# Optimization experiments

Measured on AMD Instinct MI355X. Metric: run time of the kernel, lower is better.

## Reference

```python
import jax, jax.numpy as jnp
import numpy as np
import math

QK_DIM = 128

def setup_inputs() -> dict:
    key = jax.random.key(0)
    kx, kq, kk, kv = jax.random.split(key, 4)
    B, S, D, H = 4, 4096, 1024, 128
    X = jax.random.normal(kx, (B, S, D), dtype=jnp.float32)
    # xavier-normal-ish scale for weights
    std = math.sqrt(2.0 / (D + H))
    W_q = jax.random.normal(kq, (D, H), dtype=jnp.float32) * std
    W_k = jax.random.normal(kk, (D, H), dtype=jnp.float32) * std
    W_v = jax.random.normal(kv, (D, H), dtype=jnp.float32) * std
    return {"X": X, "W_q": W_q, "W_k": W_k, "W_v": W_v}

def reference(X, W_q, W_k, W_v):
    # X: [B, S, D]; single-head causal attention
    Q = X @ W_q                       # [B, S, H]
    K = X @ W_k                       # [B, S, H]
    V = X @ W_v                       # [B, S, H]
    S_len = X.shape[1]
    scores = jnp.einsum('bsh,bth->bst', Q, K) / math.sqrt(QK_DIM)  # [B, S, S]
    causal = jnp.tril(jnp.ones((S_len, S_len), dtype=bool))
    scores = jnp.where(causal, scores, -jnp.inf)
    attn = jax.nn.softmax(scores, axis=-1)
    return jnp.einsum('bst,bth->bsh', attn, V)
```

## Files before the change

kernel.cpp:

```cpp
#include <hip/hip_runtime.h>
#include <hip/hip_bf16.h>

#define B_ 4
#define S_ 4096
#define D_ 1024
#define H_ 128

typedef unsigned short u16;
typedef unsigned int u32;
typedef short s16x8 __attribute__((ext_vector_type(8)));
typedef float f32x4 __attribute__((ext_vector_type(4)));

__device__ __forceinline__ u16 f2bf(float f) {
    u32 x = __float_as_uint(f);
    u32 r = x + 0x7fffu + ((x >> 16) & 1u);
    return (u16)(r >> 16);
}

__device__ __forceinline__ void gl_lds16(const u16* g, u16* l) {
    __builtin_amdgcn_global_load_lds(
        (const __attribute__((address_space(1))) u32*)g,
        (__attribute__((address_space(3))) u32*)l, 16, 0, 0);
}

__global__ void detect_dtype_kernel(const u32* __restrict__ w, int* __restrict__ flag) {
    __shared__ int smax[256];
    const int tid = threadIdx.x;
    int m = 0;
    for (int i = tid; i < 1024; i += 256) {
        u32 x = w[i];
        m = max(m, max((int)((x >> 7) & 0xFF), (int)((x >> 23) & 0xFF)));
    }
    smax[tid] = m;
    __syncthreads();
    if (tid == 0) {
        int mm = 0;
        for (int i = 0; i < 256; ++i) mm = max(mm, smax[i]);
        *flag = (mm >= 200) ? 1 : 0;
    }
}

__global__ __launch_bounds__(256) void prep_w_kernel(
    const void* __restrict__ Wq, const void* __restrict__ Wk, const void* __restrict__ Wv,
    u16* __restrict__ Wt, const int* __restrict__ dflag)
{
    const int kt = blockIdx.x, mat = blockIdx.y;
    const void* W = (mat == 0) ? Wq : (mat == 1) ? Wk : Wv;
    const int isf = *dflag;
    const int t = threadIdx.x;
    const int kk = t >> 3;
    const int n0 = (t & 7) * 16;
    u16 vals[16];
    if (isf) {
        const float* wp = (const float*)W + (size_t)(kt * 32 + kk) * H_ + n0;
#pragma unroll
        for (int i = 0; i < 16; ++i) vals[i] = f2bf(wp[i]);
    } else {
        const u16* wp = (const u16*)W + (size_t)(kt * 32 + kk) * H_ + n0;
#pragma unroll
        for (int i = 0; i < 16; ++i) vals[i] = wp[i];
    }
    const size_t base = (size_t)(mat * 32 + kt) * 128;
#pragma unroll
    for (int i = 0; i < 16; ++i)
        Wt[(base + n0 + i) * 32 + kk] = vals[i];
}

__global__ __launch_bounds__(256) void qkv_kernel(
    const void* __restrict__ Xv, const u16* __restrict__ Wt,
    u16* __restrict__ Qo, u16* __restrict__ Ko, u16* __restrict__ Vto,
    const int* __restrict__ dflag)
{
    __shared__ u16 Ws[2][384 * 32];
    __shared__ union { u16 qk[32 * 136]; u16 vt[128 * 40]; } OsU;

    const int isf = *dflag;
    const int tid = threadIdx.x;
    const int w = tid >> 6, lane = tid & 63;
    const int r = lane & 15, q = lane >> 4;
    const size_t m0 = (size_t)blockIdx.x * 32;

    f32x4 acc[2][6];
#pragma unroll
    for (int s2 = 0; s2 < 2; ++s2)
#pragma unroll
        for (int i = 0; i < 6; ++i) acc[s2][i] = (f32x4){0.f, 0.f, 0.f, 0.f};

    const float* xf0 = (const float*)Xv + (m0 + r) * D_;
    const float* xf1 = (const float*)Xv + (m0 + 16 + r) * D_;
    const u16*   xb0 = (const u16*)Xv + (m0 + r) * D_;
    const u16*   xb1 = (const u16*)Xv + (m0 + 16 + r) * D_;

    float4 af[2][2];
    uint4  ab[2];

#pragma unroll
    for (int i = 0; i < 6; ++i) {
        int c = tid + i * 256;
        gl_lds16(Wt + (size_t)((c >> 9) * 32) * 4096 + (c & 511) * 8, &Ws[0][c * 8]);
    }
    if (isf) {
        af[0][0] = *(const float4*)(xf0 + q * 8);
        af[0][1] = *(const float4*)(xf0 + q * 8 + 4);
        af[1][0] = *(const float4*)(xf1 + q * 8);
        af[1][1] = *(const float4*)(xf1 + q * 8 + 4);
    } else {
        ab[0] = *(const uint4*)(xb0 + q * 8);
        ab[1] = *(const uint4*)(xb1 + q * 8);
    }

    for (int kt = 0; kt < 32; ++kt) {
        const int buf = kt & 1;
        __syncthreads();

        if (kt + 1 < 32) {
#pragma unroll
            for (int i = 0; i < 6; ++i) {
                int c = tid + i * 256;
                gl_lds16(Wt + (size_t)((c >> 9) * 32 + kt + 1) * 4096 + (c & 511) * 8,
                         &Ws[buf ^ 1][c * 8]);
            }
        }

        s16x8 a[2];
        if (isf) {
#pragma unroll
            for (int s2 = 0; s2 < 2; ++s2) {
                union { u16 u[8]; s16x8 v; } pk;
                pk.u[0] = f2bf(af[s2][0].x); pk.u[1] = f2bf(af[s2][0].y);
                pk.u[2] = f2bf(af[s2][0].z); pk.u[3] = f2bf(af[s2][0].w);
                pk.u[4] = f2bf(af[s2][1].x); pk.u[5] = f2bf(af[s2][1].y);
                pk.u[6] = f2bf(af[s2][1].z); pk.u[7] = f2bf(af[s2][1].w);
                a[s2] = pk.v;
            }
        } else {
            a[0] = *(const s16x8*)&ab[0];
            a[1] = *(const s16x8*)&ab[1];
        }

        if (kt + 1 < 32) {
            const int k0 = (kt + 1) * 32;
            if (isf) {
                af[0][0] = *(const float4*)(xf0 + k0 + q * 8);
                af[0][1] = *(const float4*)(xf0 + k0 + q * 8 + 4);
                af[1][0] = *(const float4*)(xf1 + k0 + q * 8);
                af[1][1] = *(const float4*)(xf1 + k0 + q * 8 + 4);
            } else {
                ab[0] = *(const uint4*)(xb0 + k0 + q * 8);
                ab[1] = *(const uint4*)(xb1 + k0 + q * 8);
            }
        }

#pragma unroll
        for (int i = 0; i < 6; ++i) {
            int c = w * 6 + i;
            s16x8 b = *(const s16x8*)&Ws[buf][(c >> 3) * 4096 + ((c & 7) * 16 + r) * 32 + q * 8];
            acc[0][i] = __builtin_amdgcn_mfma_f32_16x16x32_bf16(a[0], b, acc[0][i], 0, 0, 0);
            acc[1][i] = __builtin_amdgcn_mfma_f32_16x16x32_bf16(a[1], b, acc[1][i], 0, 0, 0);
        }
    }

    u16* outs[2] = {Qo, Ko};
    for (int m = 0; m < 2; ++m) {
        const float sc = (m == 0) ? 0.08838834764831845f : 1.0f;
        __syncthreads();
#pragma unroll
        for (int i = 0; i < 6; ++i) {
            int c = w * 6 + i;
            if ((c >> 3) == m) {
                int nt = c & 7;
#pragma unroll
                for (int s2 = 0; s2 < 2; ++s2)
#pragma unroll
                    for (int reg = 0; reg < 4; ++reg)
                        OsU.qk[(s2 * 16 + q * 4 + reg) * 136 + nt * 16 + r] = f2bf(acc[s2][i][reg] * sc);
            }
        }
        __syncthreads();
        u16* Out = outs[m];
#pragma unroll
        for (int it = 0; it < 2; ++it) {
            int c = tid + it * 256;
            int row = c >> 4, col = (c & 15) * 8;
            *(uint4*)(Out + (m0 + row) * H_ + col) = *(const uint4*)&OsU.qk[row * 136 + col];
        }
    }

    __syncthreads();
#pragma unroll
    for (int i = 0; i < 6; ++i) {
        int c = w * 6 + i;
        if ((c >> 3) == 2) {
            int nt = c & 7;
#pragma unroll
            for (int s2 = 0; s2 < 2; ++s2)
#pragma unroll
                for (int reg = 0; reg < 4; ++reg)
                    OsU.vt[(nt * 16 + r) * 40 + s2 * 16 + q * 4 + reg] = f2bf(acc[s2][i][reg]);
        }
    }
    __syncthreads();
    {
        const int bb = blockIdx.x >> 7;
        const int s0 = (blockIdx.x & 127) * 32;
#pragma unroll
        for (int it = 0; it < 2; ++it) {
            int c = tid + it * 256;
            int h = c >> 2, sh = (c & 3) * 8;
            *(uint4*)(Vto + ((size_t)bb * H_ + h) * S_ + s0 + sh) =
                *(const uint4*)&OsU.vt[h * 40 + sh];
        }
    }
}

__global__ __launch_bounds__(256) void attn_kernel(
    const u16* __restrict__ Q, const u16* __restrict__ K, const u16* __restrict__ Vt,
    void* __restrict__ out, const int* __restrict__ dflag)
{
    __shared__ union {
        u16 ps[2][32 * 136];
        float of[32 * 132];
    } U;
    __shared__ float lsumS[4][32];

    const int isf = *dflag;
    const int tid = threadIdx.x;
    const int w = tid >> 6, lane = tid & 63;
    const int r = lane & 15, q = lane >> 4;
    const int bid = blockIdx.x;
    const int b = bid & 3;
    const int qt = (bid < 256) ? (bid >> 2) : (127 - ((bid - 256) >> 2));

    const u16* Qg  = Q  + ((size_t)b * S_ + (size_t)qt * 32) * H_;
    const u16* Kg  = K  + (size_t)b * S_ * H_;
    const u16* Vtg = Vt + (size_t)b * H_ * S_;

    s16x8 qf[2][4];
#pragma unroll
    for (int M = 0; M < 2; ++M)
#pragma unroll
        for (int ks = 0; ks < 4; ++ks)
            qf[M][ks] = *(const s16x8*)(Qg + (size_t)(M * 16 + r) * H_ + ks * 32 + q * 8);

    float lp[2][4];
#pragma unroll
    for (int M = 0; M < 2; ++M)
#pragma unroll
        for (int reg = 0; reg < 4; ++reg) lp[M][reg] = 0.f;

    f32x4 accO[2][2];
#pragma unroll
    for (int M = 0; M < 2; ++M)
#pragma unroll
        for (int ht = 0; ht < 2; ++ht) accO[M][ht] = (f32x4){0.f, 0.f, 0.f, 0.f};

    const int nKT = (qt >> 2) + 1;

    s16x8 kf[2][4];
#pragma unroll
    for (int t2 = 0; t2 < 2; ++t2)
#pragma unroll
        for (int ks = 0; ks < 4; ++ks)
            kf[t2][ks] = *(const s16x8*)(Kg + (size_t)(w * 32 + t2 * 16 + r) * H_ + ks * 32 + q * 8);

    for (int j = 0; j < nKT; ++j) {
        f32x4 accS[2][2];
#pragma unroll
        for (int M = 0; M < 2; ++M)
#pragma unroll
            for (int t2 = 0; t2 < 2; ++t2) accS[M][t2] = (f32x4){0.f, 0.f, 0.f, 0.f};
#pragma unroll
        for (int ks = 0; ks < 4; ++ks)
#pragma unroll
            for (int t2 = 0; t2 < 2; ++t2)
#pragma unroll
                for (int M = 0; M < 2; ++M)
                    accS[M][t2] = __builtin_amdgcn_mfma_f32_16x16x32_bf16(qf[M][ks], kf[t2][ks], accS[M][t2], 0, 0, 0);

        s16x8 vf[2][4];
#pragma unroll
        for (int ht = 0; ht < 2; ++ht)
#pragma unroll
            for (int ks = 0; ks < 4; ++ks)
                vf[ht][ks] = *(const s16x8*)(Vtg + (size_t)(w * 32 + ht * 16 + r) * S_ + (size_t)j * 128 + ks * 32 + q * 8);

        const bool last = (j == nKT - 1);
        const int key0 = j * 128 + w * 32 + r;
        u16* psb = &U.ps[j & 1][0];
#pragma unroll
        for (int M = 0; M < 2; ++M)
#pragma unroll
            for (int t2 = 0; t2 < 2; ++t2)
#pragma unroll
                for (int reg = 0; reg < 4; ++reg) {
                    int key = key0 + t2 * 16;
                    int grow = qt * 32 + M * 16 + q * 4 + reg;
                    float s = fminf(accS[M][t2][reg], 80.f);
                    float p = __expf(s);
                    if (last && key > grow) p = 0.f;
                    lp[M][reg] += p;
                    psb[(M * 16 + q * 4 + reg) * 136 + w * 32 + t2 * 16 + r] = f2bf(p);
                }
        __syncthreads();

        if (j + 1 < nKT) {
#pragma unroll
            for (int t2 = 0; t2 < 2; ++t2)
#pragma unroll
                for (int ks = 0; ks < 4; ++ks)
                    kf[t2][ks] = *(const s16x8*)(Kg + ((size_t)(j + 1) * 128 + w * 32 + t2 * 16 + r) * H_ + ks * 32 + q * 8);
        }

#pragma unroll
        for (int ks = 0; ks < 4; ++ks) {
            s16x8 pa0 = *(const s16x8*)&psb[(size_t)(r) * 136 + ks * 32 + q * 8];
            s16x8 pa1 = *(const s16x8*)&psb[(size_t)(16 + r) * 136 + ks * 32 + q * 8];
#pragma unroll
            for (int ht = 0; ht < 2; ++ht) {
                accO[0][ht] = __builtin_amdgcn_mfma_f32_16x16x32_bf16(pa0, vf[ht][ks], accO[0][ht], 0, 0, 0);
                accO[1][ht] = __builtin_amdgcn_mfma_f32_16x16x32_bf16(pa1, vf[ht][ks], accO[1][ht], 0, 0, 0);
            }
        }
    }

#pragma unroll
    for (int M = 0; M < 2; ++M)
#pragma unroll
        for (int reg = 0; reg < 4; ++reg) {
            float v = lp[M][reg];
            v += __shfl_xor(v, 1);
            v += __shfl_xor(v, 2);
            v += __shfl_xor(v, 4);
            v += __shfl_xor(v, 8);
            lp[M][reg] = v;
        }
    if (r == 0) {
#pragma unroll
        for (int M = 0; M < 2; ++M)
#pragma unroll
            for (int reg = 0; reg < 4; ++reg)
                lsumS[w][M * 16 + q * 4 + reg] = lp[M][reg];
    }
    __syncthreads();

    float linv[2][4];
#pragma unroll
    for (int M = 0; M < 2; ++M)
#pragma unroll
        for (int reg = 0; reg < 4; ++reg) {
            int row = M * 16 + q * 4 + reg;
            linv[M][reg] = 1.0f / (lsumS[0][row] + lsumS[1][row] + lsumS[2][row] + lsumS[3][row]);
        }

#pragma unroll
    for (int M = 0; M < 2; ++M)
#pragma unroll
        for (int ht = 0; ht < 2; ++ht)
#pragma unroll
            for (int reg = 0; reg < 4; ++reg)
                U.of[(M * 16 + q * 4 + reg) * 132 + w * 32 + ht * 16 + r] = accO[M][ht][reg] * linv[M][reg];
    __syncthreads();
    {
        const size_t obase = (size_t)b * S_ + (size_t)qt * 32;
        int row = tid >> 3, col = (tid & 7) * 16;
        const float* src = &U.of[row * 132 + col];
        if (isf) {
            float* dst = (float*)out + (obase + row) * H_ + col;
#pragma unroll
            for (int i = 0; i < 4; ++i)
                *(float4*)(dst + i * 4) = *(const float4*)(src + i * 4);
        } else {
            u16* dst = (u16*)out + (obase + row) * H_ + col;
#pragma unroll
            for (int hh = 0; hh < 2; ++hh) {
                union { u16 u[8]; uint4 v; } pk;
#pragma unroll
                for (int i = 0; i < 8; ++i) pk.u[i] = f2bf(src[hh * 8 + i]);
                *(uint4*)(dst + hh * 8) = pk.v;
            }
        }
    }
}

extern "C" void kernel_launch(void* const* d_in, const int* in_sizes, int n_in,
                              void* d_out, int out_size, void* d_ws, size_t ws_size,
                              hipStream_t stream) {
    (void)in_sizes; (void)n_in; (void)out_size; (void)ws_size;
    const void* X  = d_in[0];
    const void* Wq = d_in[1];
    const void* Wk = d_in[2];
    const void* Wv = d_in[3];

    int* dflag = (int*)d_ws;
    u16* Qw = (u16*)((char*)d_ws + 256);
    const size_t n = (size_t)B_ * S_ * H_;
    u16* Kw = Qw + n;
    u16* Vtw = Kw + n;
    u16* Wt = Vtw + n;

    detect_dtype_kernel<<<1, 256, 0, stream>>>((const u32*)Wq, dflag);
    prep_w_kernel<<<dim3(32, 3), 256, 0, stream>>>(Wq, Wk, Wv, Wt, dflag);
    qkv_kernel<<<512, 256, 0, stream>>>(X, Wt, Qw, Kw, Vtw, dflag);
    attn_kernel<<<512, 256, 0, stream>>>(Qw, Kw, Vtw, d_out, dflag);
}
```

Baseline: 213.0 us.

## Widen attention blocks to 8 waves processing 256-key tiles per iteration

The attention kernel now launches 512 threads (8 waves) per block and walks the keys in 256-wide tiles instead of 128. Each wave computes scores for 32 keys and owns a 16-column slice of the 128-wide head dimension for the PV product. This halves the number of loop iterations and block-wide barriers per query tile and puts more waves per CU. The cost is a larger LDS probability buffer, a register cap from launch_bounds(512,4), and more masked-out work in the last causal tile.

```diff
diff --git a/kernel.cpp b/kernel.cpp
--- a/kernel.cpp
+++ b/kernel.cpp
@@ -213,15 +213,15 @@
     }
 }
 
-__global__ __launch_bounds__(256) void attn_kernel(
+__global__ __launch_bounds__(512, 4) void attn_kernel(
     const u16* __restrict__ Q, const u16* __restrict__ K, const u16* __restrict__ Vt,
     void* __restrict__ out, const int* __restrict__ dflag)
 {
     __shared__ union {
-        u16 ps[2][32 * 136];
+        u16 ps[2][32 * 264];
         float of[32 * 132];
     } U;
-    __shared__ float lsumS[4][32];
+    __shared__ float lsumS[8][32];
 
     const int isf = *dflag;
     const int tid = threadIdx.x;
@@ -248,13 +248,11 @@
 #pragma unroll
         for (int reg = 0; reg < 4; ++reg) lp[M][reg] = 0.f;
 
-    f32x4 accO[2][2];
-#pragma unroll
-    for (int M = 0; M < 2; ++M)
-#pragma unroll
-        for (int ht = 0; ht < 2; ++ht) accO[M][ht] = (f32x4){0.f, 0.f, 0.f, 0.f};
-
-    const int nKT = (qt >> 2) + 1;
+    f32x4 accO[2];
+#pragma unroll
+    for (int M = 0; M < 2; ++M) accO[M] = (f32x4){0.f, 0.f, 0.f, 0.f};
+
+    const int nKT = (qt >> 3) + 1;
 
     s16x8 kf[2][4];
 #pragma unroll
@@ -277,15 +275,13 @@
                 for (int M = 0; M < 2; ++M)
                     accS[M][t2] = __builtin_amdgcn_mfma_f32_16x16x32_bf16(qf[M][ks], kf[t2][ks], accS[M][t2], 0, 0, 0);
 
-        s16x8 vf[2][4];
-#pragma unroll
-        for (int ht = 0; ht < 2; ++ht)
-#pragma unroll
-            for (int ks = 0; ks < 4; ++ks)
-                vf[ht][ks] = *(const s16x8*)(Vtg + (size_t)(w * 32 + ht * 16 + r) * S_ + (size_t)j * 128 + ks * 32 + q * 8);
+        s16x8 vf[8];
+#pragma unroll
+        for (int ks = 0; ks < 8; ++ks)
+            vf[ks] = *(const s16x8*)(Vtg + (size_t)(w * 16 + r) * S_ + (size_t)j * 256 + ks * 32 + q * 8);
 
         const bool last = (j == nKT - 1);
-        const int key0 = j * 128 + w * 32 + r;
+        const int key0 = j * 256 + w * 32 + r;
         u16* psb = &U.ps[j & 1][0];
 #pragma unroll
         for (int M = 0; M < 2; ++M)
@@ -299,7 +295,7 @@
                     float p = __expf(s);
                     if (last && key > grow) p = 0.f;
                     lp[M][reg] += p;
-                    psb[(M * 16 + q * 4 + reg) * 136 + w * 32 + t2 * 16 + r] = f2bf(p);
+                    psb[(M * 16 + q * 4 + reg) * 264 + w * 32 + t2 * 16 + r] = f2bf(p);
                 }
         __syncthreads();
 
@@ -308,18 +304,15 @@
             for (int t2 = 0; t2 < 2; ++t2)
 #pragma unroll
                 for (int ks = 0; ks < 4; ++ks)
-                    kf[t2][ks] = *(const s16x8*)(Kg + ((size_t)(j + 1) * 128 + w * 32 + t2 * 16 + r) * H_ + ks * 32 + q * 8);
-        }
-
-#pragma unroll
-        for (int ks = 0; ks < 4; ++ks) {
-            s16x8 pa0 = *(const s16x8*)&psb[(size_t)(r) * 136 + ks * 32 + q * 8];
-            s16x8 pa1 = *(const s16x8*)&psb[(size_t)(16 + r) * 136 + ks * 32 + q * 8];
-#pragma unroll
-            for (int ht = 0; ht < 2; ++ht) {
-                accO[0][ht] = __builtin_amdgcn_mfma_f32_16x16x32_bf16(pa0, vf[ht][ks], accO[0][ht], 0, 0, 0);
-                accO[1][ht] = __builtin_amdgcn_mfma_f32_16x16x32_bf16(pa1, vf[ht][ks], accO[1][ht], 0, 0, 0);
-            }
+                    kf[t2][ks] = *(const s16x8*)(Kg + ((size_t)(j + 1) * 256 + w * 32 + t2 * 16 + r) * H_ + ks * 32 + q * 8);
+        }
+
+#pragma unroll
+        for (int ks = 0; ks < 8; ++ks) {
+            s16x8 pa0 = *(const s16x8*)&psb[(size_t)(r) * 264 + ks * 32 + q * 8];
+            s16x8 pa1 = *(const s16x8*)&psb[(size_t)(16 + r) * 264 + ks * 32 + q * 8];
+            accO[0] = __builtin_amdgcn_mfma_f32_16x16x32_bf16(pa0, vf[ks], accO[0], 0, 0, 0);
+            accO[1] = __builtin_amdgcn_mfma_f32_16x16x32_bf16(pa1, vf[ks], accO[1], 0, 0, 0);
         }
     }
 
@@ -349,35 +342,33 @@
 #pragma unroll
         for (int reg = 0; reg < 4; ++reg) {
             int row = M * 16 + q * 4 + reg;
-            linv[M][reg] = 1.0f / (lsumS[0][row] + lsumS[1][row] + lsumS[2][row] + lsumS[3][row]);
-        }
-
-#pragma unroll
-    for (int M = 0; M < 2; ++M)
-#pragma unroll
-        for (int ht = 0; ht < 2; ++ht)
-#pragma unroll
-            for (int reg = 0; reg < 4; ++reg)
-                U.of[(M * 16 + q * 4 + reg) * 132 + w * 32 + ht * 16 + r] = accO[M][ht][reg] * linv[M][reg];
+            float s = 0.f;
+#pragma unroll
+            for (int ww = 0; ww < 8; ++ww) s += lsumS[ww][row];
+            linv[M][reg] = 1.0f / s;
+        }
+
+#pragma unroll
+    for (int M = 0; M < 2; ++M)
+#pragma unroll
+        for (int reg = 0; reg < 4; ++reg)
+            U.of[(M * 16 + q * 4 + reg) * 132 + w * 16 + r] = accO[M][reg] * linv[M][reg];
     __syncthreads();
     {
         const size_t obase = (size_t)b * S_ + (size_t)qt * 32;
-        int row = tid >> 3, col = (tid & 7) * 16;
+        int row = tid >> 4, col = (tid & 15) * 8;
         const float* src = &U.of[row * 132 + col];
         if (isf) {
             float* dst = (float*)out + (obase + row) * H_ + col;
 #pragma unroll
-            for (int i = 0; i < 4; ++i)
+            for (int i = 0; i < 2; ++i)
                 *(float4*)(dst + i * 4) = *(const float4*)(src + i * 4);
         } else {
             u16* dst = (u16*)out + (obase + row) * H_ + col;
-#pragma unroll
-            for (int hh = 0; hh < 2; ++hh) {
-                union { u16 u[8]; uint4 v; } pk;
-#pragma unroll
-                for (int i = 0; i < 8; ++i) pk.u[i] = f2bf(src[hh * 8 + i]);
-                *(uint4*)(dst + hh * 8) = pk.v;
-            }
+            union { u16 u[8]; uint4 v; } pk;
+#pragma unroll
+            for (int i = 0; i < 8; ++i) pk.u[i] = f2bf(src[i]);
+            *(uint4*)dst = pk.v;
         }
     }
 }
@@ -401,5 +392,5 @@
     detect_dtype_kernel<<<1, 256, 0, stream>>>((const u32*)Wq, dflag);
     prep_w_kernel<<<dim3(32, 3), 256, 0, stream>>>(Wq, Wk, Wv, Wt, dflag);
     qkv_kernel<<<512, 256, 0, stream>>>(X, Wt, Qw, Kw, Vtw, dflag);
-    attn_kernel<<<512, 256, 0, stream>>>(Qw, Kw, Vtw, d_out, dflag);
-}
+    attn_kernel<<<512, 512, 0, stream>>>(Qw, Kw, Vtw, d_out, dflag);
+}
```

Result: slower. 242.2 us (+13.7%).

## Split causal attention into balanced key-range chunks with separate combine kernel

Applied to the files above, without the earlier changes.

Replaces the single attention kernel with a split-K scheme. Each block handles a paired short/long query tile over one of four key-tile ranges, so every block does roughly the same amount of work. Unnormalized fp32 partial outputs and row sums go to workspace, and a new combine kernel sums them and normalizes. The aim is better load balance and more blocks (1024) across the CUs. The cost is extra global traffic for the fp32 partials, plus one more kernel launch.

```diff
diff --git a/kernel.cpp b/kernel.cpp
--- a/kernel.cpp
+++ b/kernel.cpp
@@ -213,171 +213,216 @@
     }
 }
 
-__global__ __launch_bounds__(256) void attn_kernel(
+__global__ __launch_bounds__(256) void attn_partial_kernel(
     const u16* __restrict__ Q, const u16* __restrict__ K, const u16* __restrict__ Vt,
-    void* __restrict__ out, const int* __restrict__ dflag)
+    float* __restrict__ OP, float* __restrict__ LP)
 {
-    __shared__ union {
-        u16 ps[2][32 * 136];
-        float of[32 * 132];
-    } U;
+    __shared__ u16 ps[2][32 * 136];
     __shared__ float lsumS[4][32];
 
-    const int isf = *dflag;
     const int tid = threadIdx.x;
     const int w = tid >> 6, lane = tid & 63;
     const int r = lane & 15, q = lane >> 4;
     const int bid = blockIdx.x;
     const int b = bid & 3;
-    const int qt = (bid < 256) ? (bid >> 2) : (127 - ((bid - 256) >> 2));
-
-    const u16* Qg  = Q  + ((size_t)b * S_ + (size_t)qt * 32) * H_;
+    const int c = (bid >> 2) & 3;
+    const int p = bid >> 4;
+    const int nA = (p >> 2) + 1;
+    const int s_c = (c == 0) ? 0 : (8 * c + 1);
+    const int e_c = 8 * c + 9;
+
     const u16* Kg  = K  + (size_t)b * S_ * H_;
     const u16* Vtg = Vt + (size_t)b * H_ * S_;
 
-    s16x8 qf[2][4];
-#pragma unroll
-    for (int M = 0; M < 2; ++M)
-#pragma unroll
-        for (int ks = 0; ks < 4; ++ks)
-            qf[M][ks] = *(const s16x8*)(Qg + (size_t)(M * 16 + r) * H_ + ks * 32 + q * 8);
-
-    float lp[2][4];
-#pragma unroll
-    for (int M = 0; M < 2; ++M)
-#pragma unroll
-        for (int reg = 0; reg < 4; ++reg) lp[M][reg] = 0.f;
-
-    f32x4 accO[2][2];
-#pragma unroll
-    for (int M = 0; M < 2; ++M)
-#pragma unroll
-        for (int ht = 0; ht < 2; ++ht) accO[M][ht] = (f32x4){0.f, 0.f, 0.f, 0.f};
-
-    const int nKT = (qt >> 2) + 1;
-
-    s16x8 kf[2][4];
-#pragma unroll
-    for (int t2 = 0; t2 < 2; ++t2)
-#pragma unroll
-        for (int ks = 0; ks < 4; ++ks)
-            kf[t2][ks] = *(const s16x8*)(Kg + (size_t)(w * 32 + t2 * 16 + r) * H_ + ks * 32 + q * 8);
-
-    for (int j = 0; j < nKT; ++j) {
-        f32x4 accS[2][2];
+    for (int seg = 0; seg < 2; ++seg) {
+        int qt, jlo, jhi;
+        if (seg == 0) {
+            if (s_c >= nA) continue;
+            qt = p; jlo = s_c; jhi = min(e_c, nA);
+        } else {
+            if (e_c <= nA) continue;
+            qt = 127 - p; jlo = max(s_c, nA) - nA; jhi = e_c - nA;
+        }
+        const int nQT = (qt >> 2) + 1;
+        const u16* Qg = Q + ((size_t)b * S_ + (size_t)qt * 32) * H_;
+
+        s16x8 qf[2][4];
 #pragma unroll
         for (int M = 0; M < 2; ++M)
 #pragma unroll
-            for (int t2 = 0; t2 < 2; ++t2) accS[M][t2] = (f32x4){0.f, 0.f, 0.f, 0.f};
-#pragma unroll
-        for (int ks = 0; ks < 4; ++ks)
-#pragma unroll
-            for (int t2 = 0; t2 < 2; ++t2)
-#pragma unroll
-                for (int M = 0; M < 2; ++M)
-                    accS[M][t2] = __builtin_amdgcn_mfma_f32_16x16x32_bf16(qf[M][ks], kf[t2][ks], accS[M][t2], 0, 0, 0);
-
-        s16x8 vf[2][4];
-#pragma unroll
-        for (int ht = 0; ht < 2; ++ht)
-#pragma unroll
             for (int ks = 0; ks < 4; ++ks)
-                vf[ht][ks] = *(const s16x8*)(Vtg + (size_t)(w * 32 + ht * 16 + r) * S_ + (size_t)j * 128 + ks * 32 + q * 8);
-
-        const bool last = (j == nKT - 1);
-        const int key0 = j * 128 + w * 32 + r;
-        u16* psb = &U.ps[j & 1][0];
+                qf[M][ks] = *(const s16x8*)(Qg + (size_t)(M * 16 + r) * H_ + ks * 32 + q * 8);
+
+        float lp[2][4];
 #pragma unroll
         for (int M = 0; M < 2; ++M)
 #pragma unroll
-            for (int t2 = 0; t2 < 2; ++t2)
-#pragma unroll
-                for (int reg = 0; reg < 4; ++reg) {
-                    int key = key0 + t2 * 16;
-                    int grow = qt * 32 + M * 16 + q * 4 + reg;
-                    float s = fminf(accS[M][t2][reg], 80.f);
-                    float p = __expf(s);
-                    if (last && key > grow) p = 0.f;
-                    lp[M][reg] += p;
-                    psb[(M * 16 + q * 4 + reg) * 136 + w * 32 + t2 * 16 + r] = f2bf(p);
+            for (int reg = 0; reg < 4; ++reg) lp[M][reg] = 0.f;
+
+        f32x4 accO[2][2];
+#pragma unroll
+        for (int M = 0; M < 2; ++M)
+#pragma unroll
+            for (int ht = 0; ht < 2; ++ht) accO[M][ht] = (f32x4){0.f, 0.f, 0.f, 0.f};
+
+        s16x8 kf[2][4];
+#pragma unroll
+        for (int t2 = 0; t2 < 2; ++t2)
+#pragma unroll
+            for (int ks = 0; ks < 4; ++ks)
+                kf[t2][ks] = *(const s16x8*)(Kg + ((size_t)jlo * 128 + w * 32 + t2 * 16 + r) * H_ + ks * 32 + q * 8);
+
+        for (int j = jlo; j < jhi; ++j) {
+            f32x4 accS[2][2];
+#pragma unroll
+            for (int M = 0; M < 2; ++M)
+#pragma unroll
+                for (int t2 = 0; t2 < 2; ++t2) accS[M][t2] = (f32x4){0.f, 0.f, 0.f, 0.f};
+#pragma unroll
+            for (int ks = 0; ks < 4; ++ks)
+#pragma unroll
+                for (int t2 = 0; t2 < 2; ++t2)
+#pragma unroll
+                    for (int M = 0; M < 2; ++M)
+                        accS[M][t2] = __builtin_amdgcn_mfma_f32_16x16x32_bf16(qf[M][ks], kf[t2][ks], accS[M][t2], 0, 0, 0);
+
+            s16x8 vf[2][4];
+#pragma unroll
+            for (int ht = 0; ht < 2; ++ht)
+#pragma unroll
+                for (int ks = 0; ks < 4; ++ks)
+                    vf[ht][ks] = *(const s16x8*)(Vtg + (size_t)(w * 32 + ht * 16 + r) * S_ + (size_t)j * 128 + ks * 32 + q * 8);
+
+            const bool last = (j == nQT - 1);
+            const int key0 = j * 128 + w * 32 + r;
+            u16* psb = &ps[j & 1][0];
+#pragma unroll
+            for (int M = 0; M < 2; ++M)
+#pragma unroll
+                for (int t2 = 0; t2 < 2; ++t2)
+#pragma unroll
+                    for (int reg = 0; reg < 4; ++reg) {
+                        int key = key0 + t2 * 16;
+                        int grow = qt * 32 + M * 16 + q * 4 + reg;
+                        float s = fminf(accS[M][t2][reg], 80.f);
+                        float pv = __expf(s);
+                        if (last && key > grow) pv = 0.f;
+                        lp[M][reg] += pv;
+                        psb[(M * 16 + q * 4 + reg) * 136 + w * 32 + t2 * 16 + r] = f2bf(pv);
+                    }
+            __syncthreads();
+
+            if (j + 1 < jhi) {
+#pragma unroll
+                for (int t2 = 0; t2 < 2; ++t2)
+#pragma unroll
+                    for (int ks = 0; ks < 4; ++ks)
+                        kf[t2][ks] = *(const s16x8*)(Kg + ((size_t)(j + 1) * 128 + w * 32 + t2 * 16 + r) * H_ + ks * 32 + q * 8);
+            }
+
+#pragma unroll
+            for (int ks = 0; ks < 4; ++ks) {
+                s16x8 pa0 = *(const s16x8*)&psb[(size_t)(r) * 136 + ks * 32 + q * 8];
+                s16x8 pa1 = *(const s16x8*)&psb[(size_t)(16 + r) * 136 + ks * 32 + q * 8];
+#pragma unroll
+                for (int ht = 0; ht < 2; ++ht) {
+                    accO[0][ht] = __builtin_amdgcn_mfma_f32_16x16x32_bf16(pa0, vf[ht][ks], accO[0][ht], 0, 0, 0);
+                    accO[1][ht] = __builtin_amdgcn_mfma_f32_16x16x32_bf16(pa1, vf[ht][ks], accO[1][ht], 0, 0, 0);
                 }
+            }
+        }
+
+#pragma unroll
+        for (int M = 0; M < 2; ++M)
+#pragma unroll
+            for (int reg = 0; reg < 4; ++reg) {
+                float v = lp[M][reg];
+                v += __shfl_xor(v, 1);
+                v += __shfl_xor(v, 2);
+                v += __shfl_xor(v, 4);
+                v += __shfl_xor(v, 8);
+                lp[M][reg] = v;
+            }
+        if (r == 0) {
+#pragma unroll
+            for (int M = 0; M < 2; ++M)
+#pragma unroll
+                for (int reg = 0; reg < 4; ++reg)
+                    lsumS[w][M * 16 + q * 4 + reg] = lp[M][reg];
+        }
         __syncthreads();
 
-        if (j + 1 < nKT) {
-#pragma unroll
-            for (int t2 = 0; t2 < 2; ++t2)
-#pragma unroll
-                for (int ks = 0; ks < 4; ++ks)
-                    kf[t2][ks] = *(const s16x8*)(Kg + ((size_t)(j + 1) * 128 + w * 32 + t2 * 16 + r) * H_ + ks * 32 + q * 8);
-        }
-
-#pragma unroll
-        for (int ks = 0; ks < 4; ++ks) {
-            s16x8 pa0 = *(const s16x8*)&psb[(size_t)(r) * 136 + ks * 32 + q * 8];
-            s16x8 pa1 = *(const s16x8*)&psb[(size_t)(16 + r) * 136 + ks * 32 + q * 8];
-#pragma unroll
-            for (int ht = 0; ht < 2; ++ht) {
-                accO[0][ht] = __builtin_amdgcn_mfma_f32_16x16x32_bf16(pa0, vf[ht][ks], accO[0][ht], 0, 0, 0);
-                accO[1][ht] = __builtin_amdgcn_mfma_f32_16x16x32_bf16(pa1, vf[ht][ks], accO[1][ht], 0, 0, 0);
-            }
-        }
-    }
-
-#pragma unroll
-    for (int M = 0; M < 2; ++M)
-#pragma unroll
-        for (int reg = 0; reg < 4; ++reg) {
-            float v = lp[M][reg];
-            v += __shfl_xor(v, 1);
-            v += __shfl_xor(v, 2);
-            v += __shfl_xor(v, 4);
-            v += __shfl_xor(v, 8);
-            lp[M][reg] = v;
-        }
-    if (r == 0) {
+        const size_t slot = (size_t)(b * 128 + qt) * 4 + c;
+        if (w == 0 && lane < 32)
+            LP[slot * 32 + lane] = lsumS[0][lane] + lsumS[1][lane] + lsumS[2][lane] + lsumS[3][lane];
+
+        float* Os = OP + slot * 32 * 128;
 #pragma unroll
         for (int M = 0; M < 2; ++M)
 #pragma unroll
-            for (int reg = 0; reg < 4; ++reg)
-                lsumS[w][M * 16 + q * 4 + reg] = lp[M][reg];
-    }
-    __syncthreads();
-
-    float linv[2][4];
-#pragma unroll
-    for (int M = 0; M < 2; ++M)
-#pragma unroll
-        for (int reg = 0; reg < 4; ++reg) {
-            int row = M * 16 + q * 4 + reg;
-            linv[M][reg] = 1.0f / (lsumS[0][row] + lsumS[1][row] + lsumS[2][row] + lsumS[3][row]);
-        }
-
-#pragma unroll
-    for (int M = 0; M < 2; ++M)
-#pragma unroll
-        for (int ht = 0; ht < 2; ++ht)
-#pragma unroll
-            for (int reg = 0; reg < 4; ++reg)
-                U.of[(M * 16 + q * 4 + reg) * 132 + w * 32 + ht * 16 + r] = accO[M][ht][reg] * linv[M][reg];
-    __syncthreads();
-    {
-        const size_t obase = (size_t)b * S_ + (size_t)qt * 32;
-        int row = tid >> 3, col = (tid & 7) * 16;
-        const float* src = &U.of[row * 132 + col];
-        if (isf) {
-            float* dst = (float*)out + (obase + row) * H_ + col;
-#pragma unroll
-            for (int i = 0; i < 4; ++i)
-                *(float4*)(dst + i * 4) = *(const float4*)(src + i * 4);
-        } else {
-            u16* dst = (u16*)out + (obase + row) * H_ + col;
-#pragma unroll
-            for (int hh = 0; hh < 2; ++hh) {
-                union { u16 u[8]; uint4 v; } pk;
-#pragma unroll
-                for (int i = 0; i < 8; ++i) pk.u[i] = f2bf(src[hh * 8 + i]);
-                *(uint4*)(dst + hh * 8) = pk.v;
-            }
+            for (int ht = 0; ht < 2; ++ht)
+#pragma unroll
+                for (int reg = 0; reg < 4; ++reg)
+                    Os[(M * 16 + q * 4 + reg) * 128 + w * 32 + ht * 16 + r] = accO[M][ht][reg];
+        __syncthreads();
+    }
+}
+
+__global__ __launch_bounds__(256) void combine_kernel(
+    const float* __restrict__ OP, const float* __restrict__ LP,
+    void* __restrict__ out, const int* __restrict__ dflag)
+{
+    const int isf = *dflag;
+    const int bid = blockIdx.x;
+    const int qt = bid & 127;
+    const int p = (qt < 64) ? qt : 127 - qt;
+    const bool isA = (qt < 64);
+    const int nA = (p >> 2) + 1;
+    const int tid = threadIdx.x;
+    const int row = tid >> 3;
+    const int col = (tid & 7) * 16;
+
+    float4 acc0 = {0, 0, 0, 0}, acc1 = {0, 0, 0, 0}, acc2 = {0, 0, 0, 0}, acc3 = {0, 0, 0, 0};
+    float l = 0.f;
+#pragma unroll
+    for (int c = 0; c < 4; ++c) {
+        const int s_c = (c == 0) ? 0 : (8 * c + 1);
+        const int e_c = 8 * c + 9;
+        const bool valid = isA ? (s_c < nA) : (e_c > nA);
+        if (valid) {
+            const size_t slot = (size_t)bid * 4 + c;
+            const float* Os = OP + (slot * 32 + row) * 128 + col;
+            float4 t0 = *(const float4*)(Os);
+            float4 t1 = *(const float4*)(Os + 4);
+            float4 t2 = *(const float4*)(Os + 8);
+            float4 t3 = *(const float4*)(Os + 12);
+            acc0.x += t0.x; acc0.y += t0.y; acc0.z += t0.z; acc0.w += t0.w;
+            acc1.x += t1.x; acc1.y += t1.y; acc1.z += t1.z; acc1.w += t1.w;
+            acc2.x += t2.x; acc2.y += t2.y; acc2.z += t2.z; acc2.w += t2.w;
+            acc3.x += t3.x; acc3.y += t3.y; acc3.z += t3.z; acc3.w += t3.w;
+            l += LP[slot * 32 + row];
+        }
+    }
+    const float inv = 1.0f / l;
+    float vals[16] = {acc0.x, acc0.y, acc0.z, acc0.w, acc1.x, acc1.y, acc1.z, acc1.w,
+                      acc2.x, acc2.y, acc2.z, acc2.w, acc3.x, acc3.y, acc3.z, acc3.w};
+#pragma unroll
+    for (int i = 0; i < 16; ++i) vals[i] *= inv;
+
+    const size_t orow = (size_t)(bid >> 7) * S_ + (size_t)qt * 32 + row;
+    if (isf) {
+        float* dst = (float*)out + orow * H_ + col;
+#pragma unroll
+        for (int i = 0; i < 4; ++i)
+            *(float4*)(dst + i * 4) = *(const float4*)(&vals[i * 4]);
+    } else {
+        u16* dst = (u16*)out + orow * H_ + col;
+#pragma unroll
+        for (int hh = 0; hh < 2; ++hh) {
+            union { u16 u[8]; uint4 v; } pk;
+#pragma unroll
+            for (int i = 0; i < 8; ++i) pk.u[i] = f2bf(vals[hh * 8 + i]);
+            *(uint4*)(dst + hh * 8) = pk.v;
         }
     }
 }
@@ -397,9 +442,12 @@
     u16* Kw = Qw + n;
     u16* Vtw = Kw + n;
     u16* Wt = Vtw + n;
+    float* OP = (float*)(Wt + 3 * 1024 * 128);
+    float* LP = OP + (size_t)4 * 128 * 4 * 32 * 128;
 
     detect_dtype_kernel<<<1, 256, 0, stream>>>((const u32*)Wq, dflag);
     prep_w_kernel<<<dim3(32, 3), 256, 0, stream>>>(Wq, Wk, Wv, Wt, dflag);
     qkv_kernel<<<512, 256, 0, stream>>>(X, Wt, Qw, Kw, Vtw, dflag);
-    attn_kernel<<<512, 256, 0, stream>>>(Qw, Kw, Vtw, d_out, dflag);
-}
+    attn_partial_kernel<<<1024, 256, 0, stream>>>(Qw, Kw, Vtw, OP, LP);
+    combine_kernel<<<512, 256, 0, stream>>>(OP, LP, d_out, dflag);
+}
```

Result: slower. 224.9 us (+5.6%).

## Pair causal query tiles and split long tiles across blocks with combine pass

Applied to the files above, without the earlier changes.

Replaces the 32-row attention kernel with 512-thread blocks covering 64-row query tiles. Each short tile is paired with its long mirror tile, and the long tile's KV range is split across two blocks so every block does equal work. The split partial outputs and row sums go to workspace in fp32, and a new combine kernel merges and normalizes them. This targets causal load imbalance and tail effects, at the cost of an extra launch, workspace traffic for the partials, and fewer total blocks (256).

```diff
diff --git a/kernel.cpp b/kernel.cpp
--- a/kernel.cpp
+++ b/kernel.cpp
@@ -213,171 +213,257 @@
     }
 }
 
-__global__ __launch_bounds__(256) void attn_kernel(
+__global__ __launch_bounds__(512) void attn_pair_kernel(
     const u16* __restrict__ Q, const u16* __restrict__ K, const u16* __restrict__ Vt,
-    void* __restrict__ out, const int* __restrict__ dflag)
+    void* __restrict__ out, float* __restrict__ OP, float* __restrict__ LP,
+    const int* __restrict__ dflag)
 {
     __shared__ union {
-        u16 ps[2][32 * 136];
-        float of[32 * 132];
+        u16 ps[2][64 * 136];
+        float of[64 * 132];
     } U;
-    __shared__ float lsumS[4][32];
+    __shared__ float lsumS[8][32];
 
     const int isf = *dflag;
     const int tid = threadIdx.x;
     const int w = tid >> 6, lane = tid & 63;
+    const int qh = w >> 2;
+    const int kw = w & 3;
     const int r = lane & 15, q = lane >> 4;
     const int bid = blockIdx.x;
     const int b = bid & 3;
-    const int qt = (bid < 256) ? (bid >> 2) : (127 - ((bid - 256) >> 2));
-
-    const u16* Qg  = Q  + ((size_t)b * S_ + (size_t)qt * 32) * H_;
+    const int p = (bid >> 2) & 31;
+    const int c = bid >> 7;
+    const int qtA = p, qtB = 63 - p;
+    const int nA = (p >> 1) + 1;
+    const int nB = ((63 - p) >> 1) + 1;
+    const int m = 17 - nA;
+
     const u16* Kg  = K  + (size_t)b * S_ * H_;
     const u16* Vtg = Vt + (size_t)b * H_ * S_;
 
-    s16x8 qf[2][4];
-#pragma unroll
-    for (int M = 0; M < 2; ++M)
-#pragma unroll
-        for (int ks = 0; ks < 4; ++ks)
-            qf[M][ks] = *(const s16x8*)(Qg + (size_t)(M * 16 + r) * H_ + ks * 32 + q * 8);
-
-    float lp[2][4];
-#pragma unroll
-    for (int M = 0; M < 2; ++M)
-#pragma unroll
-        for (int reg = 0; reg < 4; ++reg) lp[M][reg] = 0.f;
-
-    f32x4 accO[2][2];
-#pragma unroll
-    for (int M = 0; M < 2; ++M)
-#pragma unroll
-        for (int ht = 0; ht < 2; ++ht) accO[M][ht] = (f32x4){0.f, 0.f, 0.f, 0.f};
-
-    const int nKT = (qt >> 2) + 1;
-
-    s16x8 kf[2][4];
-#pragma unroll
-    for (int t2 = 0; t2 < 2; ++t2)
-#pragma unroll
-        for (int ks = 0; ks < 4; ++ks)
-            kf[t2][ks] = *(const s16x8*)(Kg + (size_t)(w * 32 + t2 * 16 + r) * H_ + ks * 32 + q * 8);
-
-    for (int j = 0; j < nKT; ++j) {
-        f32x4 accS[2][2];
+    for (int seg = 0; seg < 2; ++seg) {
+        int qt, jlo, jhi;
+        bool direct;
+        if (seg == 0) {
+            if (c != 0) continue;
+            qt = qtA; jlo = 0; jhi = nA; direct = true;
+        } else {
+            qt = qtB; jlo = (c == 0) ? 0 : m; jhi = (c == 0) ? m : nB; direct = false;
+        }
+        const int nQT = (qt >> 1) + 1;
+        const u16* Qg = Q + ((size_t)b * S_ + (size_t)qt * 64) * H_;
+
+        s16x8 qf[2][4];
 #pragma unroll
         for (int M = 0; M < 2; ++M)
 #pragma unroll
-            for (int t2 = 0; t2 < 2; ++t2) accS[M][t2] = (f32x4){0.f, 0.f, 0.f, 0.f};
-#pragma unroll
-        for (int ks = 0; ks < 4; ++ks)
-#pragma unroll
-            for (int t2 = 0; t2 < 2; ++t2)
-#pragma unroll
-                for (int M = 0; M < 2; ++M)
-                    accS[M][t2] = __builtin_amdgcn_mfma_f32_16x16x32_bf16(qf[M][ks], kf[t2][ks], accS[M][t2], 0, 0, 0);
-
-        s16x8 vf[2][4];
-#pragma unroll
-        for (int ht = 0; ht < 2; ++ht)
-#pragma unroll
             for (int ks = 0; ks < 4; ++ks)
-                vf[ht][ks] = *(const s16x8*)(Vtg + (size_t)(w * 32 + ht * 16 + r) * S_ + (size_t)j * 128 + ks * 32 + q * 8);
-
-        const bool last = (j == nKT - 1);
-        const int key0 = j * 128 + w * 32 + r;
-        u16* psb = &U.ps[j & 1][0];
+                qf[M][ks] = *(const s16x8*)(Qg + (size_t)(qh * 32 + M * 16 + r) * H_ + ks * 32 + q * 8);
+
+        float lp[2][4];
 #pragma unroll
         for (int M = 0; M < 2; ++M)
 #pragma unroll
-            for (int t2 = 0; t2 < 2; ++t2)
+            for (int reg = 0; reg < 4; ++reg) lp[M][reg] = 0.f;
+
+        f32x4 accO[2][2];
+#pragma unroll
+        for (int M = 0; M < 2; ++M)
+#pragma unroll
+            for (int ht = 0; ht < 2; ++ht) accO[M][ht] = (f32x4){0.f, 0.f, 0.f, 0.f};
+
+        s16x8 kf[2][4];
+#pragma unroll
+        for (int t2 = 0; t2 < 2; ++t2)
+#pragma unroll
+            for (int ks = 0; ks < 4; ++ks)
+                kf[t2][ks] = *(const s16x8*)(Kg + ((size_t)jlo * 128 + kw * 32 + t2 * 16 + r) * H_ + ks * 32 + q * 8);
+
+        for (int j = jlo; j < jhi; ++j) {
+            f32x4 accS[2][2];
+#pragma unroll
+            for (int M = 0; M < 2; ++M)
+#pragma unroll
+                for (int t2 = 0; t2 < 2; ++t2) accS[M][t2] = (f32x4){0.f, 0.f, 0.f, 0.f};
+#pragma unroll
+            for (int ks = 0; ks < 4; ++ks)
+#pragma unroll
+                for (int t2 = 0; t2 < 2; ++t2)
+#pragma unroll
+                    for (int M = 0; M < 2; ++M)
+                        accS[M][t2] = __builtin_amdgcn_mfma_f32_16x16x32_bf16(qf[M][ks], kf[t2][ks], accS[M][t2], 0, 0, 0);
+
+            s16x8 vf[2][4];
+#pragma unroll
+            for (int ht = 0; ht < 2; ++ht)
+#pragma unroll
+                for (int ks = 0; ks < 4; ++ks)
+                    vf[ht][ks] = *(const s16x8*)(Vtg + (size_t)(kw * 32 + ht * 16 + r) * S_ + (size_t)j * 128 + ks * 32 + q * 8);
+
+            const bool last = (j == nQT - 1);
+            const int key0 = j * 128 + kw * 32 + r;
+            u16* psb = &U.ps[j & 1][0];
+#pragma unroll
+            for (int M = 0; M < 2; ++M)
+#pragma unroll
+                for (int t2 = 0; t2 < 2; ++t2)
+#pragma unroll
+                    for (int reg = 0; reg < 4; ++reg) {
+                        int key = key0 + t2 * 16;
+                        int grow = qt * 64 + qh * 32 + M * 16 + q * 4 + reg;
+                        float s = fminf(accS[M][t2][reg], 80.f);
+                        float pv = __expf(s);
+                        if (last && key > grow) pv = 0.f;
+                        lp[M][reg] += pv;
+                        psb[(qh * 32 + M * 16 + q * 4 + reg) * 136 + kw * 32 + t2 * 16 + r] = f2bf(pv);
+                    }
+            __syncthreads();
+
+            if (j + 1 < jhi) {
+#pragma unroll
+                for (int t2 = 0; t2 < 2; ++t2)
+#pragma unroll
+                    for (int ks = 0; ks < 4; ++ks)
+                        kf[t2][ks] = *(const s16x8*)(Kg + ((size_t)(j + 1) * 128 + kw * 32 + t2 * 16 + r) * H_ + ks * 32 + q * 8);
+            }
+
+#pragma unroll
+            for (int ks = 0; ks < 4; ++ks) {
+                s16x8 pa0 = *(const s16x8*)&psb[(size_t)(qh * 32 + r) * 136 + ks * 32 + q * 8];
+                s16x8 pa1 = *(const s16x8*)&psb[(size_t)(qh * 32 + 16 + r) * 136 + ks * 32 + q * 8];
+#pragma unroll
+                for (int ht = 0; ht < 2; ++ht) {
+                    accO[0][ht] = __builtin_amdgcn_mfma_f32_16x16x32_bf16(pa0, vf[ht][ks], accO[0][ht], 0, 0, 0);
+                    accO[1][ht] = __builtin_amdgcn_mfma_f32_16x16x32_bf16(pa1, vf[ht][ks], accO[1][ht], 0, 0, 0);
+                }
+            }
+        }
+
+#pragma unroll
+        for (int M = 0; M < 2; ++M)
+#pragma unroll
+            for (int reg = 0; reg < 4; ++reg) {
+                float v = lp[M][reg];
+                v += __shfl_xor(v, 1);
+                v += __shfl_xor(v, 2);
+                v += __shfl_xor(v, 4);
+                v += __shfl_xor(v, 8);
+                lp[M][reg] = v;
+            }
+        if (r == 0) {
+#pragma unroll
+            for (int M = 0; M < 2; ++M)
+#pragma unroll
+                for (int reg = 0; reg < 4; ++reg)
+                    lsumS[w][M * 16 + q * 4 + reg] = lp[M][reg];
+        }
+        __syncthreads();
+
+        if (direct) {
+            float linv[2][4];
+#pragma unroll
+            for (int M = 0; M < 2; ++M)
 #pragma unroll
                 for (int reg = 0; reg < 4; ++reg) {
-                    int key = key0 + t2 * 16;
-                    int grow = qt * 32 + M * 16 + q * 4 + reg;
-                    float s = fminf(accS[M][t2][reg], 80.f);
-                    float p = __expf(s);
-                    if (last && key > grow) p = 0.f;
-                    lp[M][reg] += p;
-                    psb[(M * 16 + q * 4 + reg) * 136 + w * 32 + t2 * 16 + r] = f2bf(p);
+                    int row = M * 16 + q * 4 + reg;
+                    linv[M][reg] = 1.0f / (lsumS[qh * 4 + 0][row] + lsumS[qh * 4 + 1][row] +
+                                           lsumS[qh * 4 + 2][row] + lsumS[qh * 4 + 3][row]);
                 }
-        __syncthreads();
-
-        if (j + 1 < nKT) {
-#pragma unroll
-            for (int t2 = 0; t2 < 2; ++t2)
-#pragma unroll
-                for (int ks = 0; ks < 4; ++ks)
-                    kf[t2][ks] = *(const s16x8*)(Kg + ((size_t)(j + 1) * 128 + w * 32 + t2 * 16 + r) * H_ + ks * 32 + q * 8);
-        }
-
-#pragma unroll
-        for (int ks = 0; ks < 4; ++ks) {
-            s16x8 pa0 = *(const s16x8*)&psb[(size_t)(r) * 136 + ks * 32 + q * 8];
-            s16x8 pa1 = *(const s16x8*)&psb[(size_t)(16 + r) * 136 + ks * 32 + q * 8];
-#pragma unroll
-            for (int ht = 0; ht < 2; ++ht) {
-                accO[0][ht] = __builtin_amdgcn_mfma_f32_16x16x32_bf16(pa0, vf[ht][ks], accO[0][ht], 0, 0, 0);
-                accO[1][ht] = __builtin_amdgcn_mfma_f32_16x16x32_bf16(pa1, vf[ht][ks], accO[1][ht], 0, 0, 0);
-            }
-        }
-    }
-
-#pragma unroll
-    for (int M = 0; M < 2; ++M)
-#pragma unroll
-        for (int reg = 0; reg < 4; ++reg) {
-            float v = lp[M][reg];
-            v += __shfl_xor(v, 1);
-            v += __shfl_xor(v, 2);
-            v += __shfl_xor(v, 4);
-            v += __shfl_xor(v, 8);
-            lp[M][reg] = v;
-        }
-    if (r == 0) {
-#pragma unroll
-        for (int M = 0; M < 2; ++M)
-#pragma unroll
-            for (int reg = 0; reg < 4; ++reg)
-                lsumS[w][M * 16 + q * 4 + reg] = lp[M][reg];
-    }
-    __syncthreads();
-
-    float linv[2][4];
-#pragma unroll
-    for (int M = 0; M < 2; ++M)
-#pragma unroll
-        for (int reg = 0; reg < 4; ++reg) {
-            int row = M * 16 + q * 4 + reg;
-            linv[M][reg] = 1.0f / (lsumS[0][row] + lsumS[1][row] + lsumS[2][row] + lsumS[3][row]);
-        }
-
-#pragma unroll
-    for (int M = 0; M < 2; ++M)
-#pragma unroll
-        for (int ht = 0; ht < 2; ++ht)
-#pragma unroll
-            for (int reg = 0; reg < 4; ++reg)
-                U.of[(M * 16 + q * 4 + reg) * 132 + w * 32 + ht * 16 + r] = accO[M][ht][reg] * linv[M][reg];
-    __syncthreads();
-    {
-        const size_t obase = (size_t)b * S_ + (size_t)qt * 32;
-        int row = tid >> 3, col = (tid & 7) * 16;
-        const float* src = &U.of[row * 132 + col];
-        if (isf) {
-            float* dst = (float*)out + (obase + row) * H_ + col;
-#pragma unroll
-            for (int i = 0; i < 4; ++i)
-                *(float4*)(dst + i * 4) = *(const float4*)(src + i * 4);
+#pragma unroll
+            for (int M = 0; M < 2; ++M)
+#pragma unroll
+                for (int ht = 0; ht < 2; ++ht)
+#pragma unroll
+                    for (int reg = 0; reg < 4; ++reg)
+                        U.of[(qh * 32 + M * 16 + q * 4 + reg) * 132 + kw * 32 + ht * 16 + r] =
+                            accO[M][ht][reg] * linv[M][reg];
+            __syncthreads();
+            {
+                const size_t obase = (size_t)b * S_ + (size_t)qt * 64;
+                int row = tid >> 3, col = (tid & 7) * 16;
+                const float* src = &U.of[row * 132 + col];
+                if (isf) {
+                    float* dst = (float*)out + (obase + row) * H_ + col;
+#pragma unroll
+                    for (int i = 0; i < 4; ++i)
+                        *(float4*)(dst + i * 4) = *(const float4*)(src + i * 4);
+                } else {
+                    u16* dst = (u16*)out + (obase + row) * H_ + col;
+#pragma unroll
+                    for (int hh = 0; hh < 2; ++hh) {
+                        union { u16 u[8]; uint4 v; } pk;
+#pragma unroll
+                        for (int i = 0; i < 8; ++i) pk.u[i] = f2bf(src[hh * 8 + i]);
+                        *(uint4*)(dst + hh * 8) = pk.v;
+                    }
+                }
+            }
+            __syncthreads();
         } else {
-            u16* dst = (u16*)out + (obase + row) * H_ + col;
-#pragma unroll
-            for (int hh = 0; hh < 2; ++hh) {
-                union { u16 u[8]; uint4 v; } pk;
-#pragma unroll
-                for (int i = 0; i < 8; ++i) pk.u[i] = f2bf(src[hh * 8 + i]);
-                *(uint4*)(dst + hh * 8) = pk.v;
-            }
+            const size_t slot = (size_t)((b * 32 + p) * 2 + c);
+            if ((w == 0 || w == 4) && lane < 32)
+                LP[slot * 64 + qh * 32 + lane] =
+                    lsumS[qh * 4 + 0][lane] + lsumS[qh * 4 + 1][lane] +
+                    lsumS[qh * 4 + 2][lane] + lsumS[qh * 4 + 3][lane];
+            float* Os = OP + slot * 64 * 128;
+#pragma unroll
+            for (int M = 0; M < 2; ++M)
+#pragma unroll
+                for (int ht = 0; ht < 2; ++ht)
+#pragma unroll
+                    for (int reg = 0; reg < 4; ++reg)
+                        Os[(qh * 32 + M * 16 + q * 4 + reg) * 128 + kw * 32 + ht * 16 + r] =
+                            accO[M][ht][reg];
+            __syncthreads();
+        }
+    }
+}
+
+__global__ __launch_bounds__(256) void combine_kernel(
+    const float* __restrict__ OP, const float* __restrict__ LP,
+    void* __restrict__ out, const int* __restrict__ dflag)
+{
+    const int isf = *dflag;
+    const int bid = blockIdx.x;
+    const int b = bid >> 5;
+    const int qtl = bid & 31;
+    const int p = 31 - qtl;
+    const size_t s0 = (size_t)((b * 32 + p) * 2);
+    const int tid = threadIdx.x;
+    const int row = tid >> 2;
+    const int col0 = (tid & 3) * 32;
+
+    const float* O0 = OP + (s0 * 64 + row) * 128 + col0;
+    const float* O1 = OP + ((s0 + 1) * 64 + row) * 128 + col0;
+    const float l = LP[s0 * 64 + row] + LP[(s0 + 1) * 64 + row];
+    const float inv = 1.0f / l;
+
+    float vals[32];
+#pragma unroll
+    for (int i = 0; i < 8; ++i) {
+        float4 a = *(const float4*)(O0 + i * 4);
+        float4 bb = *(const float4*)(O1 + i * 4);
+        vals[i * 4 + 0] = (a.x + bb.x) * inv;
+        vals[i * 4 + 1] = (a.y + bb.y) * inv;
+        vals[i * 4 + 2] = (a.z + bb.z) * inv;
+        vals[i * 4 + 3] = (a.w + bb.w) * inv;
+    }
+
+    const size_t orow = (size_t)b * S_ + (size_t)(32 + qtl) * 64 + row;
+    if (isf) {
+        float* dst = (float*)out + orow * H_ + col0;
+#pragma unroll
+        for (int i = 0; i < 8; ++i)
+            *(float4*)(dst + i * 4) = *(const float4*)(&vals[i * 4]);
+    } else {
+        u16* dst = (u16*)out + orow * H_ + col0;
+#pragma unroll
+        for (int hh = 0; hh < 4; ++hh) {
+            union { u16 u[8]; uint4 v; } pk;
+#pragma unroll
+            for (int i = 0; i < 8; ++i) pk.u[i] = f2bf(vals[hh * 8 + i]);
+            *(uint4*)(dst + hh * 8) = pk.v;
         }
     }
 }
@@ -397,9 +483,12 @@
     u16* Kw = Qw + n;
     u16* Vtw = Kw + n;
     u16* Wt = Vtw + n;
+    float* OP = (float*)(Wt + 3 * 1024 * 128);
+    float* LP = OP + (size_t)256 * 64 * 128;
 
     detect_dtype_kernel<<<1, 256, 0, stream>>>((const u32*)Wq, dflag);
     prep_w_kernel<<<dim3(32, 3), 256, 0, stream>>>(Wq, Wk, Wv, Wt, dflag);
     qkv_kernel<<<512, 256, 0, stream>>>(X, Wt, Qw, Kw, Vtw, dflag);
-    attn_kernel<<<512, 256, 0, stream>>>(Qw, Kw, Vtw, d_out, dflag);
-}
+    attn_pair_kernel<<<256, 512, 0, stream>>>(Qw, Kw, Vtw, d_out, OP, LP, dflag);
+    combine_kernel<<<128, 256, 0, stream>>>(OP, LP, d_out, dflag);
+}
```

Result: slower. 219.7 us (+3.1%).
